# Kernel optimization log

Hardware: AMD Instinct MI355X
Metric: run time of the kernel (lower is better)

## Reference

```python
import jax, jax.numpy as jnp
import numpy as np

H = 1024  # hidden size


def lstm_layer(x, W_ih, W_hh, b_ih, b_hh):
    # x: [B, T, in] -> outputs [B, T, H]; torch gate order (i, f, g, o)
    xg = jnp.einsum('bti,gi->btg', x, W_ih) + (b_ih + b_hh)  # [B, T, 4H]
    xg = jnp.swapaxes(xg, 0, 1)  # [T, B, 4H] for scan over time
    B = x.shape[0]
    h0 = jnp.zeros((B, H), x.dtype)
    c0 = jnp.zeros((B, H), x.dtype)

    def step(carry, xg_t):
        h, c = carry
        g = xg_t + h @ W_hh.T  # [B, 4H]
        i, f, gc, o = jnp.split(g, 4, axis=-1)
        i = jax.nn.sigmoid(i)
        f = jax.nn.sigmoid(f)
        gc = jnp.tanh(gc)
        o = jax.nn.sigmoid(o)
        c = f * c + i * gc
        h = o * jnp.tanh(c)
        return (h, c), h

    (_, _), hs = jax.lax.scan(step, (h0, c0), xg)
    return jnp.swapaxes(hs, 0, 1)  # [B, T, H]


def setup_inputs() -> dict:
    key = jax.random.key(0)
    ks = jax.random.split(key, 11)
    s = 1.0 / np.sqrt(H)  # torch LSTM init scale
    return {
        'x': jax.random.normal(ks[0], (64, 512, 128), jnp.float32),
        'W_ih0': jax.random.normal(ks[1], (4 * H, 128), jnp.float32) * s,
        'W_hh0': jax.random.normal(ks[2], (4 * H, H), jnp.float32) * s,
        'b_ih0': jax.random.normal(ks[3], (4 * H,), jnp.float32) * s,
        'b_hh0': jax.random.normal(ks[4], (4 * H,), jnp.float32) * s,
        'W_ih1': jax.random.normal(ks[5], (4 * H, H), jnp.float32) * s,
        'W_hh1': jax.random.normal(ks[6], (4 * H, H), jnp.float32) * s,
        'b_ih1': jax.random.normal(ks[7], (4 * H,), jnp.float32) * s,
        'b_hh1': jax.random.normal(ks[8], (4 * H,), jnp.float32) * s,
        'fc_w': jax.random.normal(ks[9], (1, H), jnp.float32) * s,
        'fc_b': jax.random.normal(ks[10], (1,), jnp.float32) * s,
    }


def reference(x, W_ih0, W_hh0, b_ih0, b_hh0, W_ih1, W_hh1, b_ih1, b_hh1, fc_w, fc_b):
    h1 = lstm_layer(x, W_ih0, W_hh0, b_ih0, b_hh0)   # [B, T, H]
    h2 = lstm_layer(h1, W_ih1, W_hh1, b_ih1, b_hh1)  # [B, T, H]
    return h2[:, -1, :] @ fc_w.T + fc_b              # [B, 1]
```

## Files before the change

### kernel.cpp

```cpp
#include <hip/hip_runtime.h>
#include <math.h>

#define HDIM 1024
#define BDIM 64
#define TDIM 512
#define KIN  128
#define NBLK 256
#define NTHR 1024
#define FRAME (HDIM * BDIM)
#define SUBF  (HDIM * 32)

typedef _Float16 f16;
typedef __attribute__((ext_vector_type(2))) _Float16 f16x2;
typedef __attribute__((ext_vector_type(8))) _Float16 f16x8;
typedef __attribute__((ext_vector_type(4))) float f32x4;
typedef __attribute__((ext_vector_type(4))) unsigned u32x4;

#define MFMA16(a, b, c) __builtin_amdgcn_mfma_f32_16x16x32_f16((a), (b), (c), 0, 0, 0)

__device__ __forceinline__ float sigm(float x) { return 1.0f / (1.0f + expf(-x)); }

__device__ __forceinline__ f16x8 ld_cg(const f16* p) {
    f16x8 r;
    asm volatile("global_load_dwordx4 %0, %1, off sc0 sc1"
                 : "=v"(r) : "v"(p) : "memory");
    return r;
}
#define VM_WAIT4(r0, r1, r2, r3)                                         \
    asm volatile("s_waitcnt vmcnt(0)"                                    \
                 : "+v"(r0), "+v"(r1), "+v"(r2), "+v"(r3))

__device__ __forceinline__ void st_cg8(f16* p, uint2 v) {
    asm volatile("global_store_dwordx2 %0, %1, off sc0 sc1"
                 :: "v"(p), "v"(v) : "memory");
}
#define VM_DRAIN() asm volatile("s_waitcnt vmcnt(0)" ::: "memory")

__device__ __forceinline__ void tag_pub(unsigned* tag, unsigned v) {
    asm volatile("global_store_dword %0, %1, off sc0 sc1"
                 :: "v"(tag), "v"(v) : "memory");
}
__device__ __forceinline__ void tag_poll(const unsigned* tags, int lane,
                                         unsigned tgt) {
    const unsigned* p = tags + lane * 4;
    for (;;) {
        u32x4 t;
        asm volatile("global_load_dwordx4 %0, %1, off sc0 sc1\n\t"
                     "s_waitcnt vmcnt(0)"
                     : "=v"(t) : "v"(p) : "memory");
        bool ok = (t.x >= tgt) && (t.y >= tgt) && (t.z >= tgt) && (t.w >= tgt);
        if (__all(ok)) break;
        __builtin_amdgcn_s_sleep(1);
    }
}

__global__ void cvt_w(const float* __restrict__ src, f16* __restrict__ dst, int n2) {
    int i = blockIdx.x * blockDim.x + threadIdx.x;
    if (i < n2) {
        float2 a = ((const float2*)src)[i];
        f16x2 o = {(f16)a.x, (f16)a.y};
        ((f16x2*)dst)[i] = o;
    }
}

__global__ void cvt_x(const float* __restrict__ x, f16* __restrict__ xP) {
    int P = blockIdx.x * blockDim.x + threadIdx.x;
    if (P >= TDIM * BDIM * (KIN / 2)) return;
    int kp = P & 63;
    int b  = (P >> 6) & 63;
    int t  = P >> 12;
    float2 v = ((const float2*)x)[((size_t)b * TDIM + t) * (KIN / 2) + kp];
    f16x2 o = {(f16)v.x, (f16)v.y};
    ((f16x2*)xP)[((size_t)t * BDIM + b) * (KIN / 2) + kp] = o;
}

__global__ void __launch_bounds__(NTHR, 4) lstm_fused(
    const f16* __restrict__ xP,
    const f16* __restrict__ Wc0, const f16* __restrict__ Wh0,
    const float* __restrict__ bih0, const float* __restrict__ bhh0,
    const f16* __restrict__ Wc1, const f16* __restrict__ Wh1,
    const float* __restrict__ bih1, const float* __restrict__ bhh1,
    f16* ring1, f16* ring2, unsigned* tagA, unsigned* tagB) {

    __shared__ float red[32 * 324 + 16];
    __shared__ __align__(16) f16 hbuf1[32 * 8];
    __shared__ __align__(16) f16 hbuf2[32 * 8];

    const int tid  = threadIdx.x;
    const int lane = tid & 63;
    const int w    = __builtin_amdgcn_readfirstlane(tid >> 6);
    const int bid  = (int)blockIdx.x;
    const int cg   = __builtin_amdgcn_readfirstlane(bid & 127);
    const int bg   = __builtin_amdgcn_readfirstlane(bid >> 7);
    const int i0   = cg * 8;
    const int b0   = bg * 32;

    const int n    = lane & 15;
    const int quad = lane >> 4;
    const int am   = lane & 15;
    const int kq   = quad * 8;

    int wr[2];
    #pragma unroll
    for (int nt = 0; nt < 2; ++nt)
        wr[nt] = i0 + nt * 4 + (n >> 2) + (n & 3) * HDIM;

    f16x8 B1x[2];
    f16x8 B1h[2][2], B2i[2][2], B2h[2][2];
    {
        if (w < 4)
            #pragma unroll
            for (int nt = 0; nt < 2; ++nt)
                B1x[nt] = *(const f16x8*)(Wc0 + (size_t)wr[nt] * KIN + w * 32 + kq);
        #pragma unroll
        for (int j = 0; j < 2; ++j) {
            const int ks = (2 * w + j) * 32 + kq;
            #pragma unroll
            for (int nt = 0; nt < 2; ++nt) {
                B1h[j][nt] = *(const f16x8*)(Wh0 + (size_t)wr[nt] * HDIM + ks);
                B2i[j][nt] = *(const f16x8*)(Wc1 + (size_t)wr[nt] * HDIM + ks);
                B2h[j][nt] = *(const f16x8*)(Wh1 + (size_t)wr[nt] * HDIM + ks);
            }
        }
    }

    float bias1[4], bias2[4];
    float c1 = 0.f, c2 = 0.f;
    const int il   = w;
    const int cO   = il * 2 + (lane >> 5);
    const int b32O = lane & 31;
    const int mtO  = (lane >> 4) & 1;
    const int qmO  = lane & 15;
    const int ntO  = il >> 1;
    const int nbO  = ((il & 1) * 2 + (lane >> 5)) * 4;
    if (w < 4) {
        const int i = i0 + cO;
        #pragma unroll
        for (int g = 0; g < 4; ++g) {
            bias1[g] = bih0[i + g * HDIM] + bhh0[i + g * HDIM];
            bias2[g] = bih1[i + g * HDIM] + bhh1[i + g * HDIM];
        }
    }

    if (w == 8) {
        uint2 z = {0u, 0u};
        st_cg8(ring1 + FRAME + bg * SUBF + cg * 256 + lane * 4, z);
        VM_DRAIN();
        if (lane == 0) tag_pub(tagA + bid, 1u);
    }
    if (w == 9) {
        uint2 z = {0u, 0u};
        st_cg8(ring2 + FRAME + bg * SUBF + cg * 256 + lane * 4, z);
        VM_DRAIN();
        if (lane == 0) tag_pub(tagB + bid, 1u);
    }

    for (int s = 0; s <= TDIM; ++s) {
        const f16* r1p = ring1 + (size_t)((s + 1) & 1) * FRAME + bg * SUBF;
        const f16* r2p = ring2 + (size_t)(s & 1) * FRAME + bg * SUBF;

        if (w == 0) tag_poll(tagA, lane, (unsigned)(s + 1));
        __syncthreads();

        f16x8 A1[2][2];
        #pragma unroll
        for (int j = 0; j < 2; ++j) {
            const int oct = (2 * w + j) * 4 + quad;
            #pragma unroll
            for (int mt = 0; mt < 2; ++mt)
                A1[j][mt] = ld_cg(r1p + oct * 256 + (mt * 16 + am) * 8);
        }
        VM_WAIT4(A1[0][0], A1[0][1], A1[1][0], A1[1][1]);

        f32x4 acc[2][2], acc2[2][2];
        #pragma unroll
        for (int mt = 0; mt < 2; ++mt)
            #pragma unroll
            for (int nt = 0; nt < 2; ++nt) {
                acc[mt][nt]  = (f32x4){0.f, 0.f, 0.f, 0.f};
                acc2[mt][nt] = (f32x4){0.f, 0.f, 0.f, 0.f};
            }
        #pragma unroll
        for (int j = 0; j < 2; ++j)
            #pragma unroll
            for (int nt = 0; nt < 2; ++nt)
                #pragma unroll
                for (int mt = 0; mt < 2; ++mt) {
                    acc[mt][nt]  = MFMA16(A1[j][mt], B1h[j][nt], acc[mt][nt]);
                    acc2[mt][nt] = MFMA16(A1[j][mt], B2i[j][nt], acc2[mt][nt]);
                }
        if (w < 4) {
            const int ts = (s < TDIM) ? s : (TDIM - 1);
            const f16* xb = xP + (size_t)ts * BDIM * KIN;
            const int kx = w * 32 + kq;
            f16x8 ax[2];
            #pragma unroll
            for (int mt = 0; mt < 2; ++mt)
                ax[mt] = *(const f16x8*)(xb + (size_t)(b0 + mt * 16 + am) * KIN + kx);
            #pragma unroll
            for (int nt = 0; nt < 2; ++nt)
                #pragma unroll
                for (int mt = 0; mt < 2; ++mt)
                    acc[mt][nt] = MFMA16(ax[mt], B1x[nt], acc[mt][nt]);
        }

        const int p = w & 7;
        if (w < 8) {
            #pragma unroll
            for (int mt = 0; mt < 2; ++mt)
                #pragma unroll
                for (int nt = 0; nt < 2; ++nt)
                    *(f32x4*)&red[(p * 4 + mt * 2 + nt) * 324 + n * 20 + quad * 4] = acc[mt][nt];
        }
        __syncthreads();
        if (w >= 8) {
            #pragma unroll
            for (int mt = 0; mt < 2; ++mt)
                #pragma unroll
                for (int nt = 0; nt < 2; ++nt) {
                    float* a = &red[(p * 4 + mt * 2 + nt) * 324 + n * 20 + quad * 4];
                    f32x4 v = *(f32x4*)a;
                    *(f32x4*)a = v + acc[mt][nt];
                }
        }
        __syncthreads();

        if (w < 4 && s < TDIM) {
            float g4[4];
            #pragma unroll
            for (int g = 0; g < 4; ++g) {
                float sum = bias1[g];
                #pragma unroll
                for (int pp = 0; pp < 8; ++pp)
                    sum += red[(pp * 4 + mtO * 2 + ntO) * 324 + (nbO + g) * 20 + qmO];
                g4[g] = sum;
            }
            float ig = sigm(g4[0]), fg = sigm(g4[1]);
            float gg = tanhf(g4[2]), og = sigm(g4[3]);
            c1 = fg * c1 + ig * gg;
            hbuf1[b32O * 8 + cO] = (f16)(og * tanhf(c1));
        }
        if (w == 15) tag_poll(tagB, lane, (unsigned)s);
        __syncthreads();

        if (w == 8 && s < TDIM) {
            uint2 v = *(const uint2*)&hbuf1[lane * 4];
            st_cg8(ring1 + (size_t)(s & 1) * FRAME + bg * SUBF + cg * 256 + lane * 4, v);
            VM_DRAIN();
            if (lane == 0) tag_pub(tagA + bid, (unsigned)(s + 2));
        }

        f16x8 A2[2][2];
        #pragma unroll
        for (int j = 0; j < 2; ++j) {
            const int oct = (2 * w + j) * 4 + quad;
            #pragma unroll
            for (int mt = 0; mt < 2; ++mt)
                A2[j][mt] = ld_cg(r2p + oct * 256 + (mt * 16 + am) * 8);
        }
        VM_WAIT4(A2[0][0], A2[0][1], A2[1][0], A2[1][1]);
        #pragma unroll
        for (int j = 0; j < 2; ++j)
            #pragma unroll
            for (int nt = 0; nt < 2; ++nt)
                #pragma unroll
                for (int mt = 0; mt < 2; ++mt)
                    acc2[mt][nt] = MFMA16(A2[j][mt], B2h[j][nt], acc2[mt][nt]);

        if (w < 8) {
            #pragma unroll
            for (int mt = 0; mt < 2; ++mt)
                #pragma unroll
                for (int nt = 0; nt < 2; ++nt)
                    *(f32x4*)&red[(p * 4 + mt * 2 + nt) * 324 + n * 20 + quad * 4] = acc2[mt][nt];
        }
        __syncthreads();
        if (w >= 8) {
            #pragma unroll
            for (int mt = 0; mt < 2; ++mt)
                #pragma unroll
                for (int nt = 0; nt < 2; ++nt) {
                    float* a = &red[(p * 4 + mt * 2 + nt) * 324 + n * 20 + quad * 4];
                    f32x4 v = *(f32x4*)a;
                    *(f32x4*)a = v + acc2[mt][nt];
                }
        }
        __syncthreads();

        if (w < 4 && s >= 1) {
            float g4[4];
            #pragma unroll
            for (int g = 0; g < 4; ++g) {
                float sum = bias2[g];
                #pragma unroll
                for (int pp = 0; pp < 8; ++pp)
                    sum += red[(pp * 4 + mtO * 2 + ntO) * 324 + (nbO + g) * 20 + qmO];
                g4[g] = sum;
            }
            float ig = sigm(g4[0]), fg = sigm(g4[1]);
            float gg = tanhf(g4[2]), og = sigm(g4[3]);
            c2 = fg * c2 + ig * gg;
            hbuf2[b32O * 8 + cO] = (f16)(og * tanhf(c2));
        }
        __syncthreads();

        if (w == 9 && s >= 1) {
            uint2 v = *(const uint2*)&hbuf2[lane * 4];
            st_cg8(ring2 + (size_t)((s + 1) & 1) * FRAME + bg * SUBF + cg * 256 + lane * 4, v);
            VM_DRAIN();
            if (lane == 0) tag_pub(tagB + bid, (unsigned)(s + 1));
        }
    }
}

__global__ void fc_kernel(const f16* __restrict__ h2f,
                          const float* __restrict__ fcw,
                          const float* __restrict__ fcb,
                          float* __restrict__ out) {
    __shared__ float red[256];
    const int tid = threadIdx.x;
    const int b = tid >> 2, q = tid & 3;
    const int base = (b >> 5) * SUBF + (b & 31) * 8;
    float s = 0.f;
    for (int oct = q * 32; oct < (q + 1) * 32; ++oct) {
        f16x8 v = *(const f16x8*)(h2f + base + oct * 256);
        #pragma unroll
        for (int j = 0; j < 8; ++j)
            s = fmaf((float)v[j], fcw[oct * 8 + j], s);
    }
    red[tid] = s;
    __syncthreads();
    if (q == 0)
        out[b] = red[tid] + red[tid + 1] + red[tid + 2] + red[tid + 3] + fcb[0];
}

extern "C" void kernel_launch(void* const* d_in, const int* in_sizes, int n_in,
                              void* d_out, int out_size, void* d_ws, size_t ws_size,
                              hipStream_t stream) {
    const float* x    = (const float*)d_in[0];
    const float* Wih0 = (const float*)d_in[1];
    const float* Whh0 = (const float*)d_in[2];
    const float* bih0 = (const float*)d_in[3];
    const float* bhh0 = (const float*)d_in[4];
    const float* Wih1 = (const float*)d_in[5];
    const float* Whh1 = (const float*)d_in[6];
    const float* bih1 = (const float*)d_in[7];
    const float* bhh1 = (const float*)d_in[8];
    const float* fcw  = (const float*)d_in[9];
    const float* fcb  = (const float*)d_in[10];
    float* out = (float*)d_out;

    f16* xPd   = (f16*)d_ws;
    f16* Wc0   = xPd + (size_t)TDIM * BDIM * KIN;
    f16* Wh0   = Wc0 + (size_t)4 * HDIM * KIN;
    f16* Wc1   = Wh0 + (size_t)4 * HDIM * HDIM;
    f16* Wh1   = Wc1 + (size_t)4 * HDIM * HDIM;
    f16* ring1 = Wh1 + (size_t)4 * HDIM * HDIM;
    f16* ring2 = ring1 + 2 * FRAME;
    unsigned* tagA = (unsigned*)(ring2 + 2 * FRAME);
    unsigned* tagB = tagA + 512;

    hipMemsetAsync(tagA, 0, 4096, stream);
    {
        int n2 = 4 * HDIM * KIN / 2;
        cvt_w<<<dim3((n2 + 255) / 256), dim3(256), 0, stream>>>(Wih0, Wc0, n2);
        n2 = 4 * HDIM * HDIM / 2;
        cvt_w<<<dim3((n2 + 255) / 256), dim3(256), 0, stream>>>(Whh0, Wh0, n2);
        cvt_w<<<dim3((n2 + 255) / 256), dim3(256), 0, stream>>>(Whh1, Wh1, n2);
        cvt_w<<<dim3((n2 + 255) / 256), dim3(256), 0, stream>>>(Wih1, Wc1, n2);
    }
    {
        int np = TDIM * BDIM * (KIN / 2);
        cvt_x<<<dim3((np + 255) / 256), dim3(256), 0, stream>>>(x, xPd);
    }

    void* args[13];
    args[0]  = (void*)&xPd;
    args[1]  = (void*)&Wc0;
    args[2]  = (void*)&Wh0;
    args[3]  = (void*)&bih0;
    args[4]  = (void*)&bhh0;
    args[5]  = (void*)&Wc1;
    args[6]  = (void*)&Wh1;
    args[7]  = (void*)&bih1;
    args[8]  = (void*)&bhh1;
    args[9]  = (void*)&ring1;
    args[10] = (void*)&ring2;
    args[11] = (void*)&tagA;
    args[12] = (void*)&tagB;
    hipLaunchCooperativeKernel(reinterpret_cast<void*>(lstm_fused), dim3(NBLK), dim3(NTHR),
                               args, 0, stream);

    fc_kernel<<<dim3(1), dim3(256), 0, stream>>>(ring2 + FRAME, fcw, fcb, out);
}
```

Measured before the change: 3.158 ms.

## Split layers onto separate block groups with deep ring buffer pipelining

Each block previously ran both LSTM layers in lockstep. Now half the blocks run layer 0 and half run layer 1, with an 8-deep ring buffer carrying h1 between them so layer 0 can run ahead of layer 1. Each block owns 16 hidden columns with 512 threads, keeps more weights in registers, and publishes 16-byte stores. The two layers' recurrences are no longer serialized within a step, but the flag polling across roles is more complex and register pressure is higher.

```diff
diff --git a/kernel.cpp b/kernel.cpp
--- a/kernel.cpp
+++ b/kernel.cpp
@@ -6,9 +6,10 @@
 #define TDIM 512
 #define KIN  128
 #define NBLK 256
-#define NTHR 1024
+#define NTHR 512
 #define FRAME (HDIM * BDIM)
 #define SUBF  (HDIM * 32)
+#define D1    8
 
 typedef _Float16 f16;
 typedef __attribute__((ext_vector_type(2))) _Float16 f16x2;
@@ -26,23 +27,25 @@
                  : "=v"(r) : "v"(p) : "memory");
     return r;
 }
-#define VM_WAIT4(r0, r1, r2, r3)                                         \
-    asm volatile("s_waitcnt vmcnt(0)"                                    \
-                 : "+v"(r0), "+v"(r1), "+v"(r2), "+v"(r3))
-
-__device__ __forceinline__ void st_cg8(f16* p, uint2 v) {
-    asm volatile("global_store_dwordx2 %0, %1, off sc0 sc1"
+__device__ __forceinline__ void st_cg16(f16* p, u32x4 v) {
+    asm volatile("global_store_dwordx4 %0, %1, off sc0 sc1"
                  :: "v"(p), "v"(v) : "memory");
 }
-#define VM_DRAIN() asm volatile("s_waitcnt vmcnt(0)" ::: "memory")
+#define VM_WAIT_ALL()                                                    \
+    do {                                                                 \
+        asm volatile("s_waitcnt vmcnt(0)" ::: "memory");                 \
+        __builtin_amdgcn_sched_barrier(0);                               \
+    } while (0)
 
 __device__ __forceinline__ void tag_pub(unsigned* tag, unsigned v) {
     asm volatile("global_store_dword %0, %1, off sc0 sc1"
                  :: "v"(tag), "v"(v) : "memory");
 }
-__device__ __forceinline__ void tag_poll(const unsigned* tags, int lane,
-                                         unsigned tgt) {
-    const unsigned* p = tags + lane * 4;
+__device__ __forceinline__ void poll2(const unsigned* seg, int lane,
+                                      unsigned tA, unsigned tB) {
+    const int li = lane & 31;
+    const unsigned* p = seg + li * 4;
+    const unsigned tgt = (li < 16) ? tA : tB;
     for (;;) {
         u32x4 t;
         asm volatile("global_load_dwordx4 %0, %1, off sc0 sc1\n\t"
@@ -74,25 +77,26 @@
     ((f16x2*)xP)[((size_t)t * BDIM + b) * (KIN / 2) + kp] = o;
 }
 
-__global__ void __launch_bounds__(NTHR, 4) lstm_fused(
+__global__ void __launch_bounds__(NTHR) lstm_fused(
     const f16* __restrict__ xP,
     const f16* __restrict__ Wc0, const f16* __restrict__ Wh0,
     const float* __restrict__ bih0, const float* __restrict__ bhh0,
     const f16* __restrict__ Wc1, const f16* __restrict__ Wh1,
     const float* __restrict__ bih1, const float* __restrict__ bhh1,
-    f16* ring1, f16* ring2, unsigned* tagA, unsigned* tagB) {
-
-    __shared__ float red[32 * 324 + 16];
-    __shared__ __align__(16) f16 hbuf1[32 * 8];
-    __shared__ __align__(16) f16 hbuf2[32 * 8];
+    f16* ring1, f16* ring2, unsigned* tags, unsigned* tagUnused) {
+
+    __shared__ float red[64 * 324 + 16];
+    __shared__ __align__(16) f16 hbuf[32 * 16];
 
     const int tid  = threadIdx.x;
     const int lane = tid & 63;
     const int w    = __builtin_amdgcn_readfirstlane(tid >> 6);
     const int bid  = (int)blockIdx.x;
-    const int cg   = __builtin_amdgcn_readfirstlane(bid & 127);
-    const int bg   = __builtin_amdgcn_readfirstlane(bid >> 7);
-    const int i0   = cg * 8;
+    const int role = __builtin_amdgcn_readfirstlane(bid >> 7);
+    const int idx  = bid & 127;
+    const int cg   = __builtin_amdgcn_readfirstlane(idx & 63);
+    const int bg   = __builtin_amdgcn_readfirstlane(idx >> 6);
+    const int i0   = cg * 16;
     const int b0   = bg * 32;
 
     const int n    = lane & 15;
@@ -100,215 +104,211 @@
     const int am   = lane & 15;
     const int kq   = quad * 8;
 
-    int wr[2];
+    int wr[4];
     #pragma unroll
-    for (int nt = 0; nt < 2; ++nt)
+    for (int nt = 0; nt < 4; ++nt)
         wr[nt] = i0 + nt * 4 + (n >> 2) + (n & 3) * HDIM;
 
-    f16x8 B1x[2];
-    f16x8 B1h[2][2], B2i[2][2], B2h[2][2];
-    {
-        if (w < 4)
-            #pragma unroll
-            for (int nt = 0; nt < 2; ++nt)
-                B1x[nt] = *(const f16x8*)(Wc0 + (size_t)wr[nt] * KIN + w * 32 + kq);
-        #pragma unroll
-        for (int j = 0; j < 2; ++j) {
-            const int ks = (2 * w + j) * 32 + kq;
-            #pragma unroll
-            for (int nt = 0; nt < 2; ++nt) {
-                B1h[j][nt] = *(const f16x8*)(Wh0 + (size_t)wr[nt] * HDIM + ks);
-                B2i[j][nt] = *(const f16x8*)(Wc1 + (size_t)wr[nt] * HDIM + ks);
-                B2h[j][nt] = *(const f16x8*)(Wh1 + (size_t)wr[nt] * HDIM + ks);
-            }
-        }
-    }
-
-    float bias1[4], bias2[4];
-    float c1 = 0.f, c2 = 0.f;
-    const int il   = w;
-    const int cO   = il * 2 + (lane >> 5);
+    const int cO   = w * 2 + (lane >> 5);
     const int b32O = lane & 31;
     const int mtO  = (lane >> 4) & 1;
     const int qmO  = lane & 15;
-    const int ntO  = il >> 1;
-    const int nbO  = ((il & 1) * 2 + (lane >> 5)) * 4;
-    if (w < 4) {
+    const int ntO  = cO >> 2;
+    const int cit  = cO & 3;
+
+    unsigned* seg   = tags + bg * 128;
+    unsigned* mytag = seg + (role ? 64 + cg : cg);
+
+    float bias[4];
+    float cc = 0.f;
+    {
+        const float* bi = role ? bih1 : bih0;
+        const float* bh = role ? bhh1 : bhh0;
         const int i = i0 + cO;
         #pragma unroll
-        for (int g = 0; g < 4; ++g) {
-            bias1[g] = bih0[i + g * HDIM] + bhh0[i + g * HDIM];
-            bias2[g] = bih1[i + g * HDIM] + bhh1[i + g * HDIM];
-        }
-    }
-
-    if (w == 8) {
-        uint2 z = {0u, 0u};
-        st_cg8(ring1 + FRAME + bg * SUBF + cg * 256 + lane * 4, z);
-        VM_DRAIN();
-        if (lane == 0) tag_pub(tagA + bid, 1u);
-    }
-    if (w == 9) {
-        uint2 z = {0u, 0u};
-        st_cg8(ring2 + FRAME + bg * SUBF + cg * 256 + lane * 4, z);
-        VM_DRAIN();
-        if (lane == 0) tag_pub(tagB + bid, 1u);
-    }
-
-    for (int s = 0; s <= TDIM; ++s) {
-        const f16* r1p = ring1 + (size_t)((s + 1) & 1) * FRAME + bg * SUBF;
-        const f16* r2p = ring2 + (size_t)(s & 1) * FRAME + bg * SUBF;
-
-        if (w == 0) tag_poll(tagA, lane, (unsigned)(s + 1));
-        __syncthreads();
-
-        f16x8 A1[2][2];
+        for (int g = 0; g < 4; ++g)
+            bias[g] = bi[i + g * HDIM] + bh[i + g * HDIM];
+    }
+
+    if (role == 0) {
+        f16x8 B1h[4][4];
+        f16x8 B1x[4];
         #pragma unroll
-        for (int j = 0; j < 2; ++j) {
-            const int oct = (2 * w + j) * 4 + quad;
+        for (int j = 0; j < 4; ++j) {
+            const int ks = (w * 4 + j) * 32 + kq;
+            #pragma unroll
+            for (int nt = 0; nt < 4; ++nt)
+                B1h[j][nt] = *(const f16x8*)(Wh0 + (size_t)wr[nt] * HDIM + ks);
+        }
+        if (w < 4)
+            #pragma unroll
+            for (int nt = 0; nt < 4; ++nt)
+                B1x[nt] = *(const f16x8*)(Wc0 + (size_t)wr[nt] * KIN + w * 32 + kq);
+
+        if (w == 2) {
+            u32x4 z = {0u, 0u, 0u, 0u};
+            st_cg16(ring1 + (size_t)(D1 - 1) * FRAME + bg * SUBF + cg * 512 + lane * 8, z);
+            VM_WAIT_ALL();
+            if (lane == 0) tag_pub(mytag, 1u);
+        }
+
+        for (int s = 0; s < TDIM; ++s) {
+            const f16* rp = ring1 + (size_t)((s + D1 - 1) & (D1 - 1)) * FRAME + bg * SUBF;
+            if (w == 0)
+                poll2(seg, lane, (unsigned)(s + 1),
+                      (unsigned)((s >= D1) ? (s - D1 + 2) : 0));
+            __syncthreads();
+
+            f16x8 A[4][2];
+            #pragma unroll
+            for (int j = 0; j < 4; ++j) {
+                const int oct = (w * 4 + j) * 4 + quad;
+                #pragma unroll
+                for (int mt = 0; mt < 2; ++mt)
+                    A[j][mt] = ld_cg(rp + oct * 256 + (mt * 16 + am) * 8);
+            }
+            f16x8 ax[2];
+            if (w < 4) {
+                const f16* xb = xP + (size_t)s * BDIM * KIN;
+                #pragma unroll
+                for (int mt = 0; mt < 2; ++mt)
+                    ax[mt] = *(const f16x8*)(xb + (size_t)(b0 + mt * 16 + am) * KIN + w * 32 + kq);
+            }
+            VM_WAIT_ALL();
+
+            f32x4 acc[2][4];
             #pragma unroll
             for (int mt = 0; mt < 2; ++mt)
-                A1[j][mt] = ld_cg(r1p + oct * 256 + (mt * 16 + am) * 8);
-        }
-        VM_WAIT4(A1[0][0], A1[0][1], A1[1][0], A1[1][1]);
-
-        f32x4 acc[2][2], acc2[2][2];
-        #pragma unroll
-        for (int mt = 0; mt < 2; ++mt)
-            #pragma unroll
-            for (int nt = 0; nt < 2; ++nt) {
-                acc[mt][nt]  = (f32x4){0.f, 0.f, 0.f, 0.f};
-                acc2[mt][nt] = (f32x4){0.f, 0.f, 0.f, 0.f};
-            }
-        #pragma unroll
-        for (int j = 0; j < 2; ++j)
-            #pragma unroll
-            for (int nt = 0; nt < 2; ++nt)
-                #pragma unroll
-                for (int mt = 0; mt < 2; ++mt) {
-                    acc[mt][nt]  = MFMA16(A1[j][mt], B1h[j][nt], acc[mt][nt]);
-                    acc2[mt][nt] = MFMA16(A1[j][mt], B2i[j][nt], acc2[mt][nt]);
+                #pragma unroll
+                for (int nt = 0; nt < 4; ++nt)
+                    acc[mt][nt] = (f32x4){0.f, 0.f, 0.f, 0.f};
+            #pragma unroll
+            for (int j = 0; j < 4; ++j)
+                #pragma unroll
+                for (int nt = 0; nt < 4; ++nt)
+                    #pragma unroll
+                    for (int mt = 0; mt < 2; ++mt)
+                        acc[mt][nt] = MFMA16(A[j][mt], B1h[j][nt], acc[mt][nt]);
+            if (w < 4)
+                #pragma unroll
+                for (int nt = 0; nt < 4; ++nt)
+                    #pragma unroll
+                    for (int mt = 0; mt < 2; ++mt)
+                        acc[mt][nt] = MFMA16(ax[mt], B1x[nt], acc[mt][nt]);
+
+            #pragma unroll
+            for (int mt = 0; mt < 2; ++mt)
+                #pragma unroll
+                for (int nt = 0; nt < 4; ++nt)
+                    *(f32x4*)&red[(w * 8 + mt * 4 + nt) * 324 + n * 20 + quad * 4] = acc[mt][nt];
+            __syncthreads();
+
+            {
+                float g4[4];
+                #pragma unroll
+                for (int g = 0; g < 4; ++g) {
+                    float sum = bias[g];
+                    #pragma unroll
+                    for (int p = 0; p < 8; ++p)
+                        sum += red[(p * 8 + mtO * 4 + ntO) * 324 + (cit * 4 + g) * 20 + qmO];
+                    g4[g] = sum;
                 }
-        if (w < 4) {
-            const int ts = (s < TDIM) ? s : (TDIM - 1);
-            const f16* xb = xP + (size_t)ts * BDIM * KIN;
-            const int kx = w * 32 + kq;
-            f16x8 ax[2];
+                float ig = sigm(g4[0]), fg = sigm(g4[1]);
+                float gg = tanhf(g4[2]), og = sigm(g4[3]);
+                cc = fg * cc + ig * gg;
+                hbuf[((cO >> 3) * 32 + b32O) * 8 + (cO & 7)] = (f16)(og * tanhf(cc));
+            }
+            __syncthreads();
+
+            if (w == 1) {
+                u32x4 v = *(const u32x4*)&hbuf[lane * 8];
+                st_cg16(ring1 + (size_t)(s & (D1 - 1)) * FRAME + bg * SUBF + cg * 512 + lane * 8, v);
+                VM_WAIT_ALL();
+                if (lane == 0) tag_pub(mytag, (unsigned)(s + 2));
+            }
+        }
+    } else {
+        f16x8 B2[8][4];
+        {
+            const f16* mat = (w < 4) ? Wc1 : Wh1;
+            #pragma unroll
+            for (int j = 0; j < 8; ++j) {
+                const int ks = ((w & 3) * 8 + j) * 32 + kq;
+                #pragma unroll
+                for (int nt = 0; nt < 4; ++nt)
+                    B2[j][nt] = *(const f16x8*)(mat + (size_t)wr[nt] * HDIM + ks);
+            }
+        }
+
+        if (w == 2) {
+            u32x4 z = {0u, 0u, 0u, 0u};
+            st_cg16(ring2 + (size_t)FRAME + bg * SUBF + cg * 512 + lane * 8, z);
+            VM_WAIT_ALL();
+            if (lane == 0) tag_pub(mytag, 1u);
+        }
+
+        for (int t = 0; t < TDIM; ++t) {
+            const f16* r1p = ring1 + (size_t)(t & (D1 - 1)) * FRAME + bg * SUBF;
+            const f16* r2p = ring2 + (size_t)((t + 1) & 1) * FRAME + bg * SUBF;
+            if (w == 0)
+                poll2(seg, lane, (unsigned)(t + 2), (unsigned)(t + 1));
+            __syncthreads();
+
+            const f16* base = (w < 4) ? r1p : r2p;
+            f16x8 A[8][2];
+            #pragma unroll
+            for (int j = 0; j < 8; ++j) {
+                const int oct = ((w & 3) * 8 + j) * 4 + quad;
+                #pragma unroll
+                for (int mt = 0; mt < 2; ++mt)
+                    A[j][mt] = ld_cg(base + oct * 256 + (mt * 16 + am) * 8);
+            }
+            VM_WAIT_ALL();
+
+            f32x4 acc[2][4];
             #pragma unroll
             for (int mt = 0; mt < 2; ++mt)
-                ax[mt] = *(const f16x8*)(xb + (size_t)(b0 + mt * 16 + am) * KIN + kx);
-            #pragma unroll
-            for (int nt = 0; nt < 2; ++nt)
-                #pragma unroll
-                for (int mt = 0; mt < 2; ++mt)
-                    acc[mt][nt] = MFMA16(ax[mt], B1x[nt], acc[mt][nt]);
-        }
-
-        const int p = w & 7;
-        if (w < 8) {
+                #pragma unroll
+                for (int nt = 0; nt < 4; ++nt)
+                    acc[mt][nt] = (f32x4){0.f, 0.f, 0.f, 0.f};
+            #pragma unroll
+            for (int j = 0; j < 8; ++j)
+                #pragma unroll
+                for (int nt = 0; nt < 4; ++nt)
+                    #pragma unroll
+                    for (int mt = 0; mt < 2; ++mt)
+                        acc[mt][nt] = MFMA16(A[j][mt], B2[j][nt], acc[mt][nt]);
+
             #pragma unroll
             for (int mt = 0; mt < 2; ++mt)
                 #pragma unroll
-                for (int nt = 0; nt < 2; ++nt)
-                    *(f32x4*)&red[(p * 4 + mt * 2 + nt) * 324 + n * 20 + quad * 4] = acc[mt][nt];
-        }
-        __syncthreads();
-        if (w >= 8) {
-            #pragma unroll
-            for (int mt = 0; mt < 2; ++mt)
-                #pragma unroll
-                for (int nt = 0; nt < 2; ++nt) {
-                    float* a = &red[(p * 4 + mt * 2 + nt) * 324 + n * 20 + quad * 4];
-                    f32x4 v = *(f32x4*)a;
-                    *(f32x4*)a = v + acc[mt][nt];
+                for (int nt = 0; nt < 4; ++nt)
+                    *(f32x4*)&red[(w * 8 + mt * 4 + nt) * 324 + n * 20 + quad * 4] = acc[mt][nt];
+            __syncthreads();
+
+            {
+                float g4[4];
+                #pragma unroll
+                for (int g = 0; g < 4; ++g) {
+                    float sum = bias[g];
+                    #pragma unroll
+                    for (int p = 0; p < 8; ++p)
+                        sum += red[(p * 8 + mtO * 4 + ntO) * 324 + (cit * 4 + g) * 20 + qmO];
+                    g4[g] = sum;
                 }
-        }
-        __syncthreads();
-
-        if (w < 4 && s < TDIM) {
-            float g4[4];
-            #pragma unroll
-            for (int g = 0; g < 4; ++g) {
-                float sum = bias1[g];
-                #pragma unroll
-                for (int pp = 0; pp < 8; ++pp)
-                    sum += red[(pp * 4 + mtO * 2 + ntO) * 324 + (nbO + g) * 20 + qmO];
-                g4[g] = sum;
-            }
-            float ig = sigm(g4[0]), fg = sigm(g4[1]);
-            float gg = tanhf(g4[2]), og = sigm(g4[3]);
-            c1 = fg * c1 + ig * gg;
-            hbuf1[b32O * 8 + cO] = (f16)(og * tanhf(c1));
-        }
-        if (w == 15) tag_poll(tagB, lane, (unsigned)s);
-        __syncthreads();
-
-        if (w == 8 && s < TDIM) {
-            uint2 v = *(const uint2*)&hbuf1[lane * 4];
-            st_cg8(ring1 + (size_t)(s & 1) * FRAME + bg * SUBF + cg * 256 + lane * 4, v);
-            VM_DRAIN();
-            if (lane == 0) tag_pub(tagA + bid, (unsigned)(s + 2));
-        }
-
-        f16x8 A2[2][2];
-        #pragma unroll
-        for (int j = 0; j < 2; ++j) {
-            const int oct = (2 * w + j) * 4 + quad;
-            #pragma unroll
-            for (int mt = 0; mt < 2; ++mt)
-                A2[j][mt] = ld_cg(r2p + oct * 256 + (mt * 16 + am) * 8);
-        }
-        VM_WAIT4(A2[0][0], A2[0][1], A2[1][0], A2[1][1]);
-        #pragma unroll
-        for (int j = 0; j < 2; ++j)
-            #pragma unroll
-            for (int nt = 0; nt < 2; ++nt)
-                #pragma unroll
-                for (int mt = 0; mt < 2; ++mt)
-                    acc2[mt][nt] = MFMA16(A2[j][mt], B2h[j][nt], acc2[mt][nt]);
-
-        if (w < 8) {
-            #pragma unroll
-            for (int mt = 0; mt < 2; ++mt)
-                #pragma unroll
-                for (int nt = 0; nt < 2; ++nt)
-                    *(f32x4*)&red[(p * 4 + mt * 2 + nt) * 324 + n * 20 + quad * 4] = acc2[mt][nt];
-        }
-        __syncthreads();
-        if (w >= 8) {
-            #pragma unroll
-            for (int mt = 0; mt < 2; ++mt)
-                #pragma unroll
-                for (int nt = 0; nt < 2; ++nt) {
-                    float* a = &red[(p * 4 + mt * 2 + nt) * 324 + n * 20 + quad * 4];
-                    f32x4 v = *(f32x4*)a;
-                    *(f32x4*)a = v + acc2[mt][nt];
-                }
-        }
-        __syncthreads();
-
-        if (w < 4 && s >= 1) {
-            float g4[4];
-            #pragma unroll
-            for (int g = 0; g < 4; ++g) {
-                float sum = bias2[g];
-                #pragma unroll
-                for (int pp = 0; pp < 8; ++pp)
-                    sum += red[(pp * 4 + mtO * 2 + ntO) * 324 + (nbO + g) * 20 + qmO];
-                g4[g] = sum;
-            }
-            float ig = sigm(g4[0]), fg = sigm(g4[1]);
-            float gg = tanhf(g4[2]), og = sigm(g4[3]);
-            c2 = fg * c2 + ig * gg;
-            hbuf2[b32O * 8 + cO] = (f16)(og * tanhf(c2));
-        }
-        __syncthreads();
-
-        if (w == 9 && s >= 1) {
-            uint2 v = *(const uint2*)&hbuf2[lane * 4];
-            st_cg8(ring2 + (size_t)((s + 1) & 1) * FRAME + bg * SUBF + cg * 256 + lane * 4, v);
-            VM_DRAIN();
-            if (lane == 0) tag_pub(tagB + bid, (unsigned)(s + 1));
+                float ig = sigm(g4[0]), fg = sigm(g4[1]);
+                float gg = tanhf(g4[2]), og = sigm(g4[3]);
+                cc = fg * cc + ig * gg;
+                hbuf[((cO >> 3) * 32 + b32O) * 8 + (cO & 7)] = (f16)(og * tanhf(cc));
+            }
+            __syncthreads();
+
+            if (w == 1) {
+                u32x4 v = *(const u32x4*)&hbuf[lane * 8];
+                st_cg16(ring2 + (size_t)(t & 1) * FRAME + bg * SUBF + cg * 512 + lane * 8, v);
+                VM_WAIT_ALL();
+                if (lane == 0) tag_pub(mytag, (unsigned)(t + 2));
+            }
         }
     }
 }
@@ -356,11 +356,10 @@
     f16* Wc1   = Wh0 + (size_t)4 * HDIM * HDIM;
     f16* Wh1   = Wc1 + (size_t)4 * HDIM * HDIM;
     f16* ring1 = Wh1 + (size_t)4 * HDIM * HDIM;
-    f16* ring2 = ring1 + 2 * FRAME;
-    unsigned* tagA = (unsigned*)(ring2 + 2 * FRAME);
-    unsigned* tagB = tagA + 512;
-
-    hipMemsetAsync(tagA, 0, 4096, stream);
+    f16* ring2 = ring1 + (size_t)D1 * FRAME;
+    unsigned* tags = (unsigned*)(ring2 + 2 * FRAME);
+
+    hipMemsetAsync(tags, 0, 4096, stream);
     {
         int n2 = 4 * HDIM * KIN / 2;
         cvt_w<<<dim3((n2 + 255) / 256), dim3(256), 0, stream>>>(Wih0, Wc0, n2);
@@ -386,8 +385,8 @@
     args[8]  = (void*)&bhh1;
     args[9]  = (void*)&ring1;
     args[10] = (void*)&ring2;
-    args[11] = (void*)&tagA;
-    args[12] = (void*)&tagB;
+    args[11] = (void*)&tags;
+    args[12] = (void*)&tags;
     hipLaunchCooperativeKernel(reinterpret_cast<void*>(lstm_fused), dim3(NBLK), dim3(NTHR),
                                args, 0, stream);
 
```

New measurement: 3.866 ms. +22.4%, slower.

## Merge both LSTM layers' per-step phases into one barrier round with batched loads

Applied to the files above, without the earlier changes.

Both layers' recurrent inputs (ring1 and ring2) and the x slice are now loaded together, followed by a single wait. Both layers' MFMAs run in one pass and both partial sums go through one shared reduction. Gate math for layer 1 runs on waves 0-3 and for layer 2 on waves 4-7 in parallel. Tag polling now checks only the 128 blocks of the same batch group instead of all 256. This removes two __syncthreads and a separate global-load round trip per timestep, at the cost of doubling the LDS reduction buffer and adding register pressure.

```diff
diff --git a/kernel.cpp b/kernel.cpp
--- a/kernel.cpp
+++ b/kernel.cpp
@@ -14,6 +14,7 @@
 typedef __attribute__((ext_vector_type(2))) _Float16 f16x2;
 typedef __attribute__((ext_vector_type(8))) _Float16 f16x8;
 typedef __attribute__((ext_vector_type(4))) float f32x4;
+typedef __attribute__((ext_vector_type(2))) unsigned u32x2;
 typedef __attribute__((ext_vector_type(4))) unsigned u32x4;
 
 #define MFMA16(a, b, c) __builtin_amdgcn_mfma_f32_16x16x32_f16((a), (b), (c), 0, 0, 0)
@@ -26,29 +27,30 @@
                  : "=v"(r) : "v"(p) : "memory");
     return r;
 }
-#define VM_WAIT4(r0, r1, r2, r3)                                         \
-    asm volatile("s_waitcnt vmcnt(0)"                                    \
-                 : "+v"(r0), "+v"(r1), "+v"(r2), "+v"(r3))
-
 __device__ __forceinline__ void st_cg8(f16* p, uint2 v) {
     asm volatile("global_store_dwordx2 %0, %1, off sc0 sc1"
                  :: "v"(p), "v"(v) : "memory");
 }
 #define VM_DRAIN() asm volatile("s_waitcnt vmcnt(0)" ::: "memory")
+#define VM_WAIT_ALL()                                                    \
+    do {                                                                 \
+        asm volatile("s_waitcnt vmcnt(0)" ::: "memory");                 \
+        __builtin_amdgcn_sched_barrier(0);                               \
+    } while (0)
 
 __device__ __forceinline__ void tag_pub(unsigned* tag, unsigned v) {
     asm volatile("global_store_dword %0, %1, off sc0 sc1"
                  :: "v"(tag), "v"(v) : "memory");
 }
-__device__ __forceinline__ void tag_poll(const unsigned* tags, int lane,
-                                         unsigned tgt) {
-    const unsigned* p = tags + lane * 4;
+__device__ __forceinline__ void tag_poll128(const unsigned* tags, int lane,
+                                            unsigned tgt) {
+    const unsigned* p = tags + lane * 2;
     for (;;) {
-        u32x4 t;
-        asm volatile("global_load_dwordx4 %0, %1, off sc0 sc1\n\t"
+        u32x2 t;
+        asm volatile("global_load_dwordx2 %0, %1, off sc0 sc1\n\t"
                      "s_waitcnt vmcnt(0)"
                      : "=v"(t) : "v"(p) : "memory");
-        bool ok = (t.x >= tgt) && (t.y >= tgt) && (t.z >= tgt) && (t.w >= tgt);
+        bool ok = (t.x >= tgt) && (t.y >= tgt);
         if (__all(ok)) break;
         __builtin_amdgcn_s_sleep(1);
     }
@@ -82,7 +84,7 @@
     const float* __restrict__ bih1, const float* __restrict__ bhh1,
     f16* ring1, f16* ring2, unsigned* tagA, unsigned* tagB) {
 
-    __shared__ float red[32 * 324 + 16];
+    __shared__ float red[64 * 324 + 16];
     __shared__ __align__(16) f16 hbuf1[32 * 8];
     __shared__ __align__(16) f16 hbuf2[32 * 8];
 
@@ -124,22 +126,22 @@
         }
     }
 
-    float bias1[4], bias2[4];
-    float c1 = 0.f, c2 = 0.f;
-    const int il   = w;
-    const int cO   = il * 2 + (lane >> 5);
+    const int wOwn = w & 3;
+    const int cO   = wOwn * 2 + (lane >> 5);
     const int b32O = lane & 31;
     const int mtO  = (lane >> 4) & 1;
     const int qmO  = lane & 15;
-    const int ntO  = il >> 1;
-    const int nbO  = ((il & 1) * 2 + (lane >> 5)) * 4;
-    if (w < 4) {
+    const int ntO  = cO >> 2;
+    const int cit  = cO & 3;
+    float bias[4];
+    float cc = 0.f;
+    if (w < 8) {
+        const float* bi = (w < 4) ? bih0 : bih1;
+        const float* bh = (w < 4) ? bhh0 : bhh1;
         const int i = i0 + cO;
         #pragma unroll
-        for (int g = 0; g < 4; ++g) {
-            bias1[g] = bih0[i + g * HDIM] + bhh0[i + g * HDIM];
-            bias2[g] = bih1[i + g * HDIM] + bhh1[i + g * HDIM];
-        }
+        for (int g = 0; g < 4; ++g)
+            bias[g] = bi[i + g * HDIM] + bh[i + g * HDIM];
     }
 
     if (w == 8) {
@@ -159,18 +161,29 @@
         const f16* r1p = ring1 + (size_t)((s + 1) & 1) * FRAME + bg * SUBF;
         const f16* r2p = ring2 + (size_t)(s & 1) * FRAME + bg * SUBF;
 
-        if (w == 0) tag_poll(tagA, lane, (unsigned)(s + 1));
+        if (w == 0)  tag_poll128(tagA + bg * 128, lane, (unsigned)(s + 1));
+        if (w == 15) tag_poll128(tagB + bg * 128, lane, (unsigned)s);
         __syncthreads();
 
-        f16x8 A1[2][2];
+        f16x8 A1[2][2], A2[2][2];
         #pragma unroll
         for (int j = 0; j < 2; ++j) {
             const int oct = (2 * w + j) * 4 + quad;
             #pragma unroll
+            for (int mt = 0; mt < 2; ++mt) {
+                A1[j][mt] = ld_cg(r1p + oct * 256 + (mt * 16 + am) * 8);
+                A2[j][mt] = ld_cg(r2p + oct * 256 + (mt * 16 + am) * 8);
+            }
+        }
+        f16x8 ax[2];
+        if (w < 4) {
+            const int ts = (s < TDIM) ? s : (TDIM - 1);
+            const f16* xb = xP + (size_t)ts * BDIM * KIN;
+            #pragma unroll
             for (int mt = 0; mt < 2; ++mt)
-                A1[j][mt] = ld_cg(r1p + oct * 256 + (mt * 16 + am) * 8);
-        }
-        VM_WAIT4(A1[0][0], A1[0][1], A1[1][0], A1[1][1]);
+                ax[mt] = *(const f16x8*)(xb + (size_t)(b0 + mt * 16 + am) * KIN + w * 32 + kq);
+        }
+        VM_WAIT_ALL();
 
         f32x4 acc[2][2], acc2[2][2];
         #pragma unroll
@@ -188,29 +201,24 @@
                 for (int mt = 0; mt < 2; ++mt) {
                     acc[mt][nt]  = MFMA16(A1[j][mt], B1h[j][nt], acc[mt][nt]);
                     acc2[mt][nt] = MFMA16(A1[j][mt], B2i[j][nt], acc2[mt][nt]);
+                    acc2[mt][nt] = MFMA16(A2[j][mt], B2h[j][nt], acc2[mt][nt]);
                 }
-        if (w < 4) {
-            const int ts = (s < TDIM) ? s : (TDIM - 1);
-            const f16* xb = xP + (size_t)ts * BDIM * KIN;
-            const int kx = w * 32 + kq;
-            f16x8 ax[2];
-            #pragma unroll
-            for (int mt = 0; mt < 2; ++mt)
-                ax[mt] = *(const f16x8*)(xb + (size_t)(b0 + mt * 16 + am) * KIN + kx);
+        if (w < 4)
             #pragma unroll
             for (int nt = 0; nt < 2; ++nt)
                 #pragma unroll
                 for (int mt = 0; mt < 2; ++mt)
                     acc[mt][nt] = MFMA16(ax[mt], B1x[nt], acc[mt][nt]);
-        }
 
         const int p = w & 7;
         if (w < 8) {
             #pragma unroll
             for (int mt = 0; mt < 2; ++mt)
                 #pragma unroll
-                for (int nt = 0; nt < 2; ++nt)
-                    *(f32x4*)&red[(p * 4 + mt * 2 + nt) * 324 + n * 20 + quad * 4] = acc[mt][nt];
+                for (int nt = 0; nt < 2; ++nt) {
+                    *(f32x4*)&red[(p * 8 + mt * 2 + nt) * 324 + n * 20 + quad * 4] = acc[mt][nt];
+                    *(f32x4*)&red[(p * 8 + 4 + mt * 2 + nt) * 324 + n * 20 + quad * 4] = acc2[mt][nt];
+                }
         }
         __syncthreads();
         if (w >= 8) {
@@ -218,9 +226,12 @@
             for (int mt = 0; mt < 2; ++mt)
                 #pragma unroll
                 for (int nt = 0; nt < 2; ++nt) {
-                    float* a = &red[(p * 4 + mt * 2 + nt) * 324 + n * 20 + quad * 4];
-                    f32x4 v = *(f32x4*)a;
-                    *(f32x4*)a = v + acc[mt][nt];
+                    float* a1 = &red[(p * 8 + mt * 2 + nt) * 324 + n * 20 + quad * 4];
+                    float* a2 = &red[(p * 8 + 4 + mt * 2 + nt) * 324 + n * 20 + quad * 4];
+                    f32x4 v1 = *(f32x4*)a1;
+                    f32x4 v2 = *(f32x4*)a2;
+                    *(f32x4*)a1 = v1 + acc[mt][nt];
+                    *(f32x4*)a2 = v2 + acc2[mt][nt];
                 }
         }
         __syncthreads();
@@ -229,18 +240,32 @@
             float g4[4];
             #pragma unroll
             for (int g = 0; g < 4; ++g) {
-                float sum = bias1[g];
+                float sum = bias[g];
                 #pragma unroll
                 for (int pp = 0; pp < 8; ++pp)
-                    sum += red[(pp * 4 + mtO * 2 + ntO) * 324 + (nbO + g) * 20 + qmO];
+                    sum += red[(pp * 8 + mtO * 2 + ntO) * 324 + (cit * 4 + g) * 20 + qmO];
                 g4[g] = sum;
             }
             float ig = sigm(g4[0]), fg = sigm(g4[1]);
             float gg = tanhf(g4[2]), og = sigm(g4[3]);
-            c1 = fg * c1 + ig * gg;
-            hbuf1[b32O * 8 + cO] = (f16)(og * tanhf(c1));
-        }
-        if (w == 15) tag_poll(tagB, lane, (unsigned)s);
+            cc = fg * cc + ig * gg;
+            hbuf1[b32O * 8 + cO] = (f16)(og * tanhf(cc));
+        }
+        if (w >= 4 && w < 8 && s >= 1) {
+            float g4[4];
+            #pragma unroll
+            for (int g = 0; g < 4; ++g) {
+                float sum = bias[g];
+                #pragma unroll
+                for (int pp = 0; pp < 8; ++pp)
+                    sum += red[(pp * 8 + 4 + mtO * 2 + ntO) * 324 + (cit * 4 + g) * 20 + qmO];
+                g4[g] = sum;
+            }
+            float ig = sigm(g4[0]), fg = sigm(g4[1]);
+            float gg = tanhf(g4[2]), og = sigm(g4[3]);
+            cc = fg * cc + ig * gg;
+            hbuf2[b32O * 8 + cO] = (f16)(og * tanhf(cc));
+        }
         __syncthreads();
 
         if (w == 8 && s < TDIM) {
@@ -249,61 +274,6 @@
             VM_DRAIN();
             if (lane == 0) tag_pub(tagA + bid, (unsigned)(s + 2));
         }
-
-        f16x8 A2[2][2];
-        #pragma unroll
-        for (int j = 0; j < 2; ++j) {
-            const int oct = (2 * w + j) * 4 + quad;
-            #pragma unroll
-            for (int mt = 0; mt < 2; ++mt)
-                A2[j][mt] = ld_cg(r2p + oct * 256 + (mt * 16 + am) * 8);
-        }
-        VM_WAIT4(A2[0][0], A2[0][1], A2[1][0], A2[1][1]);
-        #pragma unroll
-        for (int j = 0; j < 2; ++j)
-            #pragma unroll
-            for (int nt = 0; nt < 2; ++nt)
-                #pragma unroll
-                for (int mt = 0; mt < 2; ++mt)
-                    acc2[mt][nt] = MFMA16(A2[j][mt], B2h[j][nt], acc2[mt][nt]);
-
-        if (w < 8) {
-            #pragma unroll
-            for (int mt = 0; mt < 2; ++mt)
-                #pragma unroll
-                for (int nt = 0; nt < 2; ++nt)
-                    *(f32x4*)&red[(p * 4 + mt * 2 + nt) * 324 + n * 20 + quad * 4] = acc2[mt][nt];
-        }
-        __syncthreads();
-        if (w >= 8) {
-            #pragma unroll
-            for (int mt = 0; mt < 2; ++mt)
-                #pragma unroll
-                for (int nt = 0; nt < 2; ++nt) {
-                    float* a = &red[(p * 4 + mt * 2 + nt) * 324 + n * 20 + quad * 4];
-                    f32x4 v = *(f32x4*)a;
-                    *(f32x4*)a = v + acc2[mt][nt];
-                }
-        }
-        __syncthreads();
-
-        if (w < 4 && s >= 1) {
-            float g4[4];
-            #pragma unroll
-            for (int g = 0; g < 4; ++g) {
-                float sum = bias2[g];
-                #pragma unroll
-                for (int pp = 0; pp < 8; ++pp)
-                    sum += red[(pp * 4 + mtO * 2 + ntO) * 324 + (nbO + g) * 20 + qmO];
-                g4[g] = sum;
-            }
-            float ig = sigm(g4[0]), fg = sigm(g4[1]);
-            float gg = tanhf(g4[2]), og = sigm(g4[3]);
-            c2 = fg * c2 + ig * gg;
-            hbuf2[b32O * 8 + cO] = (f16)(og * tanhf(c2));
-        }
-        __syncthreads();
-
         if (w == 9 && s >= 1) {
             uint2 v = *(const uint2*)&hbuf2[lane * 4];
             st_cg8(ring2 + (size_t)((s + 1) & 1) * FRAME + bg * SUBF + cg * 256 + lane * 4, v);
```

After: 6.742 ms. +113.5%, slower.

## Poll only own batch-group tags, single-pass LDS reduction, overlap tag publish

Applied to the files above, without the earlier changes.

Tag polling now reads only the 128 tags of the block's own batch group rather than all 256. The two-phase cross-wave reduction (store, barrier, read-add) becomes a single store of all 16 waves' partials into a doubled LDS buffer, summed by the gate waves, which removes one __syncthreads per layer per step. The x-projection loads are issued alongside the ring loads, and the layer-1 tag publish is delayed to overlap with the layer-2 ring loads. The cost is twice the LDS footprint and a longer gate-side summation loop.

```diff
diff --git a/kernel.cpp b/kernel.cpp
--- a/kernel.cpp
+++ b/kernel.cpp
@@ -14,6 +14,7 @@
 typedef __attribute__((ext_vector_type(2))) _Float16 f16x2;
 typedef __attribute__((ext_vector_type(8))) _Float16 f16x8;
 typedef __attribute__((ext_vector_type(4))) float f32x4;
+typedef __attribute__((ext_vector_type(2))) unsigned u32x2;
 typedef __attribute__((ext_vector_type(4))) unsigned u32x4;
 
 #define MFMA16(a, b, c) __builtin_amdgcn_mfma_f32_16x16x32_f16((a), (b), (c), 0, 0, 0)
@@ -40,15 +41,15 @@
     asm volatile("global_store_dword %0, %1, off sc0 sc1"
                  :: "v"(tag), "v"(v) : "memory");
 }
-__device__ __forceinline__ void tag_poll(const unsigned* tags, int lane,
-                                         unsigned tgt) {
-    const unsigned* p = tags + lane * 4;
+__device__ __forceinline__ void tag_poll128(const unsigned* tags, int lane,
+                                            unsigned tgt) {
+    const unsigned* p = tags + lane * 2;
     for (;;) {
-        u32x4 t;
-        asm volatile("global_load_dwordx4 %0, %1, off sc0 sc1\n\t"
+        u32x2 t;
+        asm volatile("global_load_dwordx2 %0, %1, off sc0 sc1\n\t"
                      "s_waitcnt vmcnt(0)"
                      : "=v"(t) : "v"(p) : "memory");
-        bool ok = (t.x >= tgt) && (t.y >= tgt) && (t.z >= tgt) && (t.w >= tgt);
+        bool ok = (t.x >= tgt) && (t.y >= tgt);
         if (__all(ok)) break;
         __builtin_amdgcn_s_sleep(1);
     }
@@ -82,7 +83,7 @@
     const float* __restrict__ bih1, const float* __restrict__ bhh1,
     f16* ring1, f16* ring2, unsigned* tagA, unsigned* tagB) {
 
-    __shared__ float red[32 * 324 + 16];
+    __shared__ float red[64 * 324 + 16];
     __shared__ __align__(16) f16 hbuf1[32 * 8];
     __shared__ __align__(16) f16 hbuf2[32 * 8];
 
@@ -126,13 +127,13 @@
 
     float bias1[4], bias2[4];
     float c1 = 0.f, c2 = 0.f;
-    const int il   = w;
+    const int il   = w & 3;
     const int cO   = il * 2 + (lane >> 5);
     const int b32O = lane & 31;
     const int mtO  = (lane >> 4) & 1;
     const int qmO  = lane & 15;
-    const int ntO  = il >> 1;
-    const int nbO  = ((il & 1) * 2 + (lane >> 5)) * 4;
+    const int ntO  = cO >> 2;
+    const int nbO  = (cO & 3) * 4;
     if (w < 4) {
         const int i = i0 + cO;
         #pragma unroll
@@ -159,7 +160,7 @@
         const f16* r1p = ring1 + (size_t)((s + 1) & 1) * FRAME + bg * SUBF;
         const f16* r2p = ring2 + (size_t)(s & 1) * FRAME + bg * SUBF;
 
-        if (w == 0) tag_poll(tagA, lane, (unsigned)(s + 1));
+        if (w == 0) tag_poll128(tagA + bg * 128, lane, (unsigned)(s + 1));
         __syncthreads();
 
         f16x8 A1[2][2];
@@ -170,7 +171,16 @@
             for (int mt = 0; mt < 2; ++mt)
                 A1[j][mt] = ld_cg(r1p + oct * 256 + (mt * 16 + am) * 8);
         }
-        VM_WAIT4(A1[0][0], A1[0][1], A1[1][0], A1[1][1]);
+        f16x8 ax[2];
+        if (w < 4) {
+            const int ts = (s < TDIM) ? s : (TDIM - 1);
+            const f16* xb = xP + (size_t)ts * BDIM * KIN;
+            #pragma unroll
+            for (int mt = 0; mt < 2; ++mt)
+                ax[mt] = *(const f16x8*)(xb + (size_t)(b0 + mt * 16 + am) * KIN + w * 32 + kq);
+        }
+        VM_DRAIN();
+        __builtin_amdgcn_sched_barrier(0);
 
         f32x4 acc[2][2], acc2[2][2];
         #pragma unroll
@@ -189,40 +199,18 @@
                     acc[mt][nt]  = MFMA16(A1[j][mt], B1h[j][nt], acc[mt][nt]);
                     acc2[mt][nt] = MFMA16(A1[j][mt], B2i[j][nt], acc2[mt][nt]);
                 }
-        if (w < 4) {
-            const int ts = (s < TDIM) ? s : (TDIM - 1);
-            const f16* xb = xP + (size_t)ts * BDIM * KIN;
-            const int kx = w * 32 + kq;
-            f16x8 ax[2];
-            #pragma unroll
-            for (int mt = 0; mt < 2; ++mt)
-                ax[mt] = *(const f16x8*)(xb + (size_t)(b0 + mt * 16 + am) * KIN + kx);
+        if (w < 4)
             #pragma unroll
             for (int nt = 0; nt < 2; ++nt)
                 #pragma unroll
                 for (int mt = 0; mt < 2; ++mt)
                     acc[mt][nt] = MFMA16(ax[mt], B1x[nt], acc[mt][nt]);
-        }
-
-        const int p = w & 7;
-        if (w < 8) {
-            #pragma unroll
-            for (int mt = 0; mt < 2; ++mt)
-                #pragma unroll
-                for (int nt = 0; nt < 2; ++nt)
-                    *(f32x4*)&red[(p * 4 + mt * 2 + nt) * 324 + n * 20 + quad * 4] = acc[mt][nt];
-        }
-        __syncthreads();
-        if (w >= 8) {
-            #pragma unroll
-            for (int mt = 0; mt < 2; ++mt)
-                #pragma unroll
-                for (int nt = 0; nt < 2; ++nt) {
-                    float* a = &red[(p * 4 + mt * 2 + nt) * 324 + n * 20 + quad * 4];
-                    f32x4 v = *(f32x4*)a;
-                    *(f32x4*)a = v + acc[mt][nt];
-                }
-        }
+
+        #pragma unroll
+        for (int mt = 0; mt < 2; ++mt)
+            #pragma unroll
+            for (int nt = 0; nt < 2; ++nt)
+                *(f32x4*)&red[(w * 4 + mt * 2 + nt) * 324 + n * 20 + quad * 4] = acc[mt][nt];
         __syncthreads();
 
         if (w < 4 && s < TDIM) {
@@ -231,7 +219,7 @@
             for (int g = 0; g < 4; ++g) {
                 float sum = bias1[g];
                 #pragma unroll
-                for (int pp = 0; pp < 8; ++pp)
+                for (int pp = 0; pp < 16; ++pp)
                     sum += red[(pp * 4 + mtO * 2 + ntO) * 324 + (nbO + g) * 20 + qmO];
                 g4[g] = sum;
             }
@@ -240,14 +228,12 @@
             c1 = fg * c1 + ig * gg;
             hbuf1[b32O * 8 + cO] = (f16)(og * tanhf(c1));
         }
-        if (w == 15) tag_poll(tagB, lane, (unsigned)s);
+        if (w == 15) tag_poll128(tagB + bg * 128, lane, (unsigned)s);
         __syncthreads();
 
         if (w == 8 && s < TDIM) {
             uint2 v = *(const uint2*)&hbuf1[lane * 4];
             st_cg8(ring1 + (size_t)(s & 1) * FRAME + bg * SUBF + cg * 256 + lane * 4, v);
-            VM_DRAIN();
-            if (lane == 0) tag_pub(tagA + bid, (unsigned)(s + 2));
         }
 
         f16x8 A2[2][2];
@@ -258,7 +244,13 @@
             for (int mt = 0; mt < 2; ++mt)
                 A2[j][mt] = ld_cg(r2p + oct * 256 + (mt * 16 + am) * 8);
         }
+        if (w == 8 && s < TDIM) {
+            asm volatile("s_waitcnt vmcnt(4)" ::: "memory");
+            if (lane == 0) tag_pub(tagA + bid, (unsigned)(s + 2));
+        }
         VM_WAIT4(A2[0][0], A2[0][1], A2[1][0], A2[1][1]);
+        __builtin_amdgcn_sched_barrier(0);
+
         #pragma unroll
         for (int j = 0; j < 2; ++j)
             #pragma unroll
@@ -267,24 +259,11 @@
                 for (int mt = 0; mt < 2; ++mt)
                     acc2[mt][nt] = MFMA16(A2[j][mt], B2h[j][nt], acc2[mt][nt]);
 
-        if (w < 8) {
-            #pragma unroll
-            for (int mt = 0; mt < 2; ++mt)
-                #pragma unroll
-                for (int nt = 0; nt < 2; ++nt)
-                    *(f32x4*)&red[(p * 4 + mt * 2 + nt) * 324 + n * 20 + quad * 4] = acc2[mt][nt];
-        }
-        __syncthreads();
-        if (w >= 8) {
-            #pragma unroll
-            for (int mt = 0; mt < 2; ++mt)
-                #pragma unroll
-                for (int nt = 0; nt < 2; ++nt) {
-                    float* a = &red[(p * 4 + mt * 2 + nt) * 324 + n * 20 + quad * 4];
-                    f32x4 v = *(f32x4*)a;
-                    *(f32x4*)a = v + acc2[mt][nt];
-                }
-        }
+        #pragma unroll
+        for (int mt = 0; mt < 2; ++mt)
+            #pragma unroll
+            for (int nt = 0; nt < 2; ++nt)
+                *(f32x4*)&red[(w * 4 + mt * 2 + nt) * 324 + n * 20 + quad * 4] = acc2[mt][nt];
         __syncthreads();
 
         if (w < 4 && s >= 1) {
@@ -293,7 +272,7 @@
             for (int g = 0; g < 4; ++g) {
                 float sum = bias2[g];
                 #pragma unroll
-                for (int pp = 0; pp < 8; ++pp)
+                for (int pp = 0; pp < 16; ++pp)
                     sum += red[(pp * 4 + mtO * 2 + ntO) * 324 + (nbO + g) * 20 + qmO];
                 g4[g] = sum;
             }
```

After: 6.475 ms. +105.0%, slower.
